# Performance work log

Measured on AMD Instinct MI355X. Metric: run time of the kernel, lower is better.

Reference implementation:

```python
import jax, jax.numpy as jnp
import numpy as np

EPS = 1e-8


def setup_inputs() -> dict:
    key = jax.random.key(0)
    k1, k2, k3 = jax.random.split(key, 3)
    B, N, M, C = 4, 4096, 16384, 256
    xyz = jax.random.normal(k1, (B * N, 3), dtype=jnp.float32)
    new_xyz = jax.random.normal(k2, (B * M, 3), dtype=jnp.float32)
    feat = jax.random.normal(k3, (B * N, C), dtype=jnp.float32)
    offset = jnp.arange(1, B + 1, dtype=jnp.int64) * N      # [4096, 8192, 12288, 16384]
    new_offset = jnp.arange(1, B + 1, dtype=jnp.int64) * M  # [16384, ..., 65536]
    return {"xyz": xyz, "new_xyz": new_xyz, "feat": feat,
            "offset": offset, "new_offset": new_offset, "k": 3}


def _interpolate(xyz_b, new_xyz_b, feat_b, k):
    # xyz_b: [B,N,3], new_xyz_b: [B,M,3], feat_b: [B,N,C]
    # pairwise squared distances via GEMM: [B,M,N]
    q2 = jnp.sum(new_xyz_b * new_xyz_b, axis=-1, keepdims=True)        # [B,M,1]
    s2 = jnp.sum(xyz_b * xyz_b, axis=-1)[:, None, :]                   # [B,1,N]
    cross = jnp.einsum('bmd,bnd->bmn', new_xyz_b, xyz_b)               # [B,M,N]
    d2 = q2 + s2 - 2.0 * cross                                         # [B,M,N]
    neg_d2, idx = jax.lax.top_k(-d2, k)                                # [B,M,k]
    dist = jnp.sqrt(jnp.maximum(-neg_d2, 1e-12))                       # euclidean, like knnquery
    dist_recip = 1.0 / (dist + EPS)
    weight = dist_recip / jnp.sum(dist_recip, axis=-1, keepdims=True)  # [B,M,k]
    gathered = jax.vmap(lambda f, i: f[i])(feat_b, idx)                # [B,M,k,C]
    return jnp.einsum('bmkc,bmk->bmc', gathered, weight)               # [B,M,C]


def reference(xyz, new_xyz, feat, offset, new_offset, k):
    B = offset.shape[0]
    N = xyz.shape[0] // B
    M = new_xyz.shape[0] // B
    C = feat.shape[1]
    # uniform offsets -> reshape into per-cloud batches
    out = _interpolate(xyz.reshape(B, N, 3), new_xyz.reshape(B, M, 3),
                       feat.reshape(B, N, C), k)
    return out.reshape(B * M, C)
```

## Files before the change

kernel.cpp:

```cpp
#include <hip/hip_runtime.h>
#include <float.h>


#define QPB   32
#define SPLIT 8
#define KEY_INIT 0x7FEFFFFFFFFFFFFFULL

__global__ void pack_pts(const float* __restrict__ xyz,
                         float4* __restrict__ pts, int total) {
    int i = blockIdx.x * blockDim.x + threadIdx.x;
    if (i < total) {
        const float sx = xyz[(size_t)i * 3 + 0];
        const float sy = xyz[(size_t)i * 3 + 1];
        const float sz = xyz[(size_t)i * 3 + 2];
        const float s2 = __fadd_rn(__fadd_rn(__fmul_rn(sx, sx), __fmul_rn(sy, sy)),
                                   __fmul_rn(sz, sz));
        pts[i] = make_float4(sx, sy, sz, s2);
    }
}

__device__ __forceinline__ double mk_key(float d2, int j) {
    unsigned long long u =
        ((unsigned long long)(unsigned)__float_as_uint(d2) << 32) | (unsigned)j;
    return __longlong_as_double(u);
}

template <int CHUNK>
__global__ __launch_bounds__(256, 8) void fp_knn_main(
    const float* __restrict__ new_xyz,
    const float4* __restrict__ pts,
    const float4* __restrict__ feat4,
    float4* __restrict__ out4,
    int N, int blocks_per_batch)
{
    __shared__ double s_k[SPLIT][QPB][3];
    __shared__ float  s_w[QPB][3];
    __shared__ int    s_j[QPB][3];

    int g = blockIdx.x;
    if (gridDim.x == 2048 && blocks_per_batch == 512) {
        const int xcd = g & 7, slot = g >> 3;
        g = (xcd >> 1) * 512 + (xcd & 1) * 256 + slot;
    }

    const int tid = threadIdx.x;
    const int q   = tid & (QPB - 1);
    const int s   = tid >> 5;
    const int b   = g / blocks_per_batch;
    const int src_base = b * N;
    const int m = g * QPB + q;

    const float qx = new_xyz[(size_t)m * 3 + 0];
    const float qy = new_xyz[(size_t)m * 3 + 1];
    const float qz = new_xyz[(size_t)m * 3 + 2];
    const float q2 = __fadd_rn(__fadd_rn(__fmul_rn(qx, qx), __fmul_rn(qy, qy)),
                               __fmul_rn(qz, qz));

    const int cbase = s * CHUNK;
    const float4* __restrict__ cp = pts + src_base + cbase;

    double k0 = __longlong_as_double(KEY_INIT);
    double k1 = k0, k2 = k0;

    #pragma unroll 8
    for (int j = 0; j < CHUNK; ++j) {
        const float4 p = cp[j];
        const float cross = __fadd_rn(
            __fadd_rn(__fmul_rn(qx, p.x), __fmul_rn(qy, p.y)),
            __fmul_rn(qz, p.z));
        const float d2 = __fadd_rn(q2, p.w) - (cross + cross);
        const double key = mk_key(d2, cbase + j);
        const double n0 = fmin(key, k0);
        const double n1 = fmin(fmax(key, k0), k1);
        const double n2 = fmin(fmax(key, k1), k2);
        k0 = n0; k1 = n1; k2 = n2;
    }

    s_k[s][q][0] = k0; s_k[s][q][1] = k1; s_k[s][q][2] = k2;
    __syncthreads();

    if (tid < QPB) {
        double m0 = __longlong_as_double(KEY_INIT), m1 = m0, m2 = m0;
        #pragma unroll
        for (int ss = 0; ss < SPLIT; ++ss) {
            #pragma unroll
            for (int r = 0; r < 3; ++r) {
                const double d = s_k[ss][tid][r];
                const double n0 = fmin(d, m0);
                const double n1 = fmin(fmax(d, m0), m1);
                const double n2 = fmin(fmax(d, m1), m2);
                m0 = n0; m1 = n1; m2 = n2;
            }
        }
        unsigned long long u0 = __double_as_longlong(m0);
        unsigned long long u1 = __double_as_longlong(m1);
        unsigned long long u2 = __double_as_longlong(m2);
        const float d0 = __uint_as_float((unsigned)(u0 >> 32));
        const float d1 = __uint_as_float((unsigned)(u1 >> 32));
        const float d2 = __uint_as_float((unsigned)(u2 >> 32));
        const float e0 = sqrtf(fmaxf(d0, 1e-12f));
        const float e1 = sqrtf(fmaxf(d1, 1e-12f));
        const float e2 = sqrtf(fmaxf(d2, 1e-12f));
        const float r0 = 1.0f / (e0 + 1e-8f);
        const float r1 = 1.0f / (e1 + 1e-8f);
        const float r2 = 1.0f / (e2 + 1e-8f);
        const float rs = r0 + r1 + r2;
        s_w[tid][0] = r0 / rs; s_w[tid][1] = r1 / rs; s_w[tid][2] = r2 / rs;
        s_j[tid][0] = (int)(u0 & 0xffffffffu);
        s_j[tid][1] = (int)(u1 & 0xffffffffu);
        s_j[tid][2] = (int)(u2 & 0xffffffffu);
    }
    __syncthreads();

    const int lane  = tid & 63;
    const int wv    = tid >> 6;
    const int qbase = g * QPB;
    #pragma unroll 2
    for (int t = 0; t < QPB / 4; ++t) {
        const int qq = wv * (QPB / 4) + t;
        const int   a0 = s_j[qq][0], a1 = s_j[qq][1], a2 = s_j[qq][2];
        const float u0 = s_w[qq][0], u1 = s_w[qq][1], u2 = s_w[qq][2];
        const float4 f0 = feat4[(size_t)(src_base + a0) * 64 + lane];
        const float4 f1 = feat4[(size_t)(src_base + a1) * 64 + lane];
        const float4 f2 = feat4[(size_t)(src_base + a2) * 64 + lane];
        float4 o;
        o.x = u0 * f0.x + u1 * f1.x + u2 * f2.x;
        o.y = u0 * f0.y + u1 * f1.y + u2 * f2.y;
        o.z = u0 * f0.z + u1 * f1.z + u2 * f2.z;
        o.w = u0 * f0.w + u1 * f1.w + u2 * f2.w;
        out4[(size_t)(qbase + qq) * 64 + lane] = o;
    }
}

__global__ void fp_knn_generic(
    const float* __restrict__ new_xyz, const float* __restrict__ xyz,
    const float* __restrict__ feat, float* __restrict__ out,
    int N, int M, int Btot)
{
    const int m = blockIdx.x * blockDim.x + threadIdx.x;
    if (m >= Btot * M) return;
    const int b = m / M;
    const int src_base = b * N;
    const float qx = new_xyz[(size_t)m * 3 + 0];
    const float qy = new_xyz[(size_t)m * 3 + 1];
    const float qz = new_xyz[(size_t)m * 3 + 2];
    const float q2 = __fadd_rn(__fadd_rn(__fmul_rn(qx, qx), __fmul_rn(qy, qy)),
                               __fmul_rn(qz, qz));
    double k0 = __longlong_as_double(KEY_INIT), k1 = k0, k2 = k0;
    for (int j = 0; j < N; ++j) {
        const float sx = xyz[(size_t)(src_base + j) * 3 + 0];
        const float sy = xyz[(size_t)(src_base + j) * 3 + 1];
        const float sz = xyz[(size_t)(src_base + j) * 3 + 2];
        const float s2 = __fadd_rn(__fadd_rn(__fmul_rn(sx, sx), __fmul_rn(sy, sy)),
                                   __fmul_rn(sz, sz));
        const float cross = __fadd_rn(
            __fadd_rn(__fmul_rn(qx, sx), __fmul_rn(qy, sy)), __fmul_rn(qz, sz));
        const float d2 = __fadd_rn(q2, s2) - (cross + cross);
        const double key = mk_key(d2, j);
        const double n0 = fmin(key, k0);
        const double n1 = fmin(fmax(key, k0), k1);
        const double n2 = fmin(fmax(key, k1), k2);
        k0 = n0; k1 = n1; k2 = n2;
    }
    unsigned long long u0 = __double_as_longlong(k0);
    unsigned long long u1 = __double_as_longlong(k1);
    unsigned long long u2 = __double_as_longlong(k2);
    const float e0 = sqrtf(fmaxf(__uint_as_float((unsigned)(u0 >> 32)), 1e-12f));
    const float e1 = sqrtf(fmaxf(__uint_as_float((unsigned)(u1 >> 32)), 1e-12f));
    const float e2 = sqrtf(fmaxf(__uint_as_float((unsigned)(u2 >> 32)), 1e-12f));
    const float r0 = 1.0f / (e0 + 1e-8f);
    const float r1 = 1.0f / (e1 + 1e-8f);
    const float r2 = 1.0f / (e2 + 1e-8f);
    const float rs = r0 + r1 + r2;
    const float w0 = r0 / rs, w1 = r1 / rs, w2 = r2 / rs;
    const int a0 = (int)(u0 & 0xffffffffu), a1 = (int)(u1 & 0xffffffffu),
              a2 = (int)(u2 & 0xffffffffu);
    const int C = 256;
    for (int c = 0; c < C; ++c) {
        out[(size_t)m * C + c] =
            w0 * feat[(size_t)(src_base + a0) * C + c] +
            w1 * feat[(size_t)(src_base + a1) * C + c] +
            w2 * feat[(size_t)(src_base + a2) * C + c];
    }
}

extern "C" void kernel_launch(void* const* d_in, const int* in_sizes, int n_in,
                              void* d_out, int out_size, void* d_ws, size_t ws_size,
                              hipStream_t stream) {
    const float* xyz     = (const float*)d_in[0];
    const float* new_xyz = (const float*)d_in[1];
    const float* feat    = (const float*)d_in[2];
    float* out = (float*)d_out;

    const int B = in_sizes[3];
    const int N = in_sizes[0] / (3 * B);
    const int M = in_sizes[1] / (3 * B);

    const size_t need = (size_t)(B * N) * sizeof(float4);
    const bool fast = (N % SPLIT == 0) && (N / SPLIT == 512) &&
                      (M % QPB == 0) && (ws_size >= need);
    if (fast) {
        pack_pts<<<(B * N + 255) / 256, 256, 0, stream>>>(xyz, (float4*)d_ws, B * N);
        const int blocks = (B * M) / QPB;
        fp_knn_main<512><<<blocks, 256, 0, stream>>>(
            new_xyz, (const float4*)d_ws, (const float4*)feat, (float4*)out,
            N, M / QPB);
    } else {
        fp_knn_generic<<<(B * M + 255) / 256, 256, 0, stream>>>(
            new_xyz, xyz, feat, out, N, M, B);
    }
}
```

Measured before the change: 234.9 us.

## Use 64-query wave-aligned blocks with wave-uniform point loads and double-buffered prefetch

Doubles queries per block to 64 so each wavefront handles one split chunk, making the candidate-point index wave-uniform (readfirstlane) so point loads can become scalar/broadcast loads. Adds a double-buffered register prefetch of point groups in the distance scan. Block size grows to 512 threads, and the XCD remap and gather loop are adjusted to match. This risks higher register pressure and lower occupancy under the 512-thread launch bounds.

```diff
diff --git a/kernel.cpp b/kernel.cpp
--- a/kernel.cpp
+++ b/kernel.cpp
@@ -2,7 +2,7 @@
 #include <float.h>
 
 
-#define QPB   32
+#define QPB   64
 #define SPLIT 8
 #define KEY_INIT 0x7FEFFFFFFFFFFFFFULL
 
@@ -26,7 +26,7 @@
 }
 
 template <int CHUNK>
-__global__ __launch_bounds__(256, 8) void fp_knn_main(
+__global__ __launch_bounds__(512, 8) void fp_knn_main(
     const float* __restrict__ new_xyz,
     const float4* __restrict__ pts,
     const float4* __restrict__ feat4,
@@ -38,14 +38,13 @@
     __shared__ int    s_j[QPB][3];
 
     int g = blockIdx.x;
-    if (gridDim.x == 2048 && blocks_per_batch == 512) {
+    if (gridDim.x == 1024 && blocks_per_batch == 256) {
         const int xcd = g & 7, slot = g >> 3;
-        g = (xcd >> 1) * 512 + (xcd & 1) * 256 + slot;
+        g = (xcd >> 1) * 256 + (xcd & 1) * 128 + slot;
     }
 
     const int tid = threadIdx.x;
     const int q   = tid & (QPB - 1);
-    const int s   = tid >> 5;
     const int b   = g / blocks_per_batch;
     const int src_base = b * N;
     const int m = g * QPB + q;
@@ -56,27 +55,46 @@
     const float q2 = __fadd_rn(__fadd_rn(__fmul_rn(qx, qx), __fmul_rn(qy, qy)),
                                __fmul_rn(qz, qz));
 
-    const int cbase = s * CHUNK;
+    const int s_u   = __builtin_amdgcn_readfirstlane(tid >> 6);
+    const int cbase = s_u * CHUNK;
     const float4* __restrict__ cp = pts + src_base + cbase;
 
     double k0 = __longlong_as_double(KEY_INIT);
     double k1 = k0, k2 = k0;
 
-    #pragma unroll 8
-    for (int j = 0; j < CHUNK; ++j) {
-        const float4 p = cp[j];
+    constexpr int G  = 4;
+    constexpr int NG = CHUNK / G;
+    float4 buf[2][G];
+
+    #pragma unroll
+    for (int t = 0; t < G; ++t) buf[0][t] = cp[t];
+
+    auto process = [&](const float4 p, int cj) {
         const float cross = __fadd_rn(
             __fadd_rn(__fmul_rn(qx, p.x), __fmul_rn(qy, p.y)),
             __fmul_rn(qz, p.z));
         const float d2 = __fadd_rn(q2, p.w) - (cross + cross);
-        const double key = mk_key(d2, cbase + j);
+        const double key = mk_key(d2, cj);
         const double n0 = fmin(key, k0);
         const double n1 = fmin(fmax(key, k0), k1);
         const double n2 = fmin(fmax(key, k1), k2);
         k0 = n0; k1 = n1; k2 = n2;
-    }
-
-    s_k[s][q][0] = k0; s_k[s][q][1] = k1; s_k[s][q][2] = k2;
+    };
+
+    #pragma unroll 2
+    for (int gi = 0; gi < NG - 1; ++gi) {
+        const float4* nx = cp + (gi + 1) * G;
+        #pragma unroll
+        for (int t = 0; t < G; ++t) buf[(gi + 1) & 1][t] = nx[t];
+        #pragma unroll
+        for (int t = 0; t < G; ++t)
+            process(buf[gi & 1][t], cbase + gi * G + t);
+    }
+    #pragma unroll
+    for (int t = 0; t < G; ++t)
+        process(buf[(NG - 1) & 1][t], cbase + (NG - 1) * G + t);
+
+    s_k[s_u][q][0] = k0; s_k[s_u][q][1] = k1; s_k[s_u][q][2] = k2;
     __syncthreads();
 
     if (tid < QPB) {
@@ -116,8 +134,8 @@
     const int wv    = tid >> 6;
     const int qbase = g * QPB;
     #pragma unroll 2
-    for (int t = 0; t < QPB / 4; ++t) {
-        const int qq = wv * (QPB / 4) + t;
+    for (int t = 0; t < QPB / SPLIT; ++t) {
+        const int qq = wv * (QPB / SPLIT) + t;
         const int   a0 = s_j[qq][0], a1 = s_j[qq][1], a2 = s_j[qq][2];
         const float u0 = s_w[qq][0], u1 = s_w[qq][1], u2 = s_w[qq][2];
         const float4 f0 = feat4[(size_t)(src_base + a0) * 64 + lane];
@@ -202,7 +220,7 @@
     if (fast) {
         pack_pts<<<(B * N + 255) / 256, 256, 0, stream>>>(xyz, (float4*)d_ws, B * N);
         const int blocks = (B * M) / QPB;
-        fp_knn_main<512><<<blocks, 256, 0, stream>>>(
+        fp_knn_main<512><<<blocks, 512, 0, stream>>>(
             new_xyz, (const float4*)d_ws, (const float4*)feat, (float4*)out,
             N, M / QPB);
     } else {
```

New measurement: 213.2 us. 1.1x faster.
